# Kernel tuning notes

Measured on AMD Instinct MI355X. Metric: run time of the kernel, lower is better.

Reference implementation:

```python
import jax, jax.numpy as jnp
import numpy as np

N_NODES = 20000
N_EDGES = 640000
IN_DIM = 256
HID = 128
N_GRAPHS = 64


def setup_inputs() -> dict:
    key = jax.random.key(0)
    ks = jax.random.split(key, 9)
    x = jax.random.normal(ks[0], (N_NODES, IN_DIM), jnp.float32)
    edge_index = jax.random.randint(ks[1], (2, N_EDGES), 0, N_NODES, dtype=jnp.int32)
    batch = jnp.sort(jax.random.randint(ks[2], (N_NODES,), 0, N_GRAPHS, dtype=jnp.int32))

    def lin(k, fan_in, fan_out):
        # torch.nn.Linear default init: U(-1/sqrt(fan_in), 1/sqrt(fan_in))
        bound = 1.0 / np.sqrt(fan_in)
        kw, kb = jax.random.split(k)
        W = jax.random.uniform(kw, (fan_in, fan_out), jnp.float32, -bound, bound)
        b = jax.random.uniform(kb, (fan_out,), jnp.float32, -bound, bound)
        return W, b

    W0, b0 = lin(ks[3], IN_DIM, HID)
    W1, b1 = lin(ks[4], HID, HID)
    W2, b2 = lin(ks[5], HID, HID)
    return dict(x=x, edge_index=edge_index, batch=batch,
                W0=W0, b0=b0, W1=W1, b1=b1, W2=W2, b2=b2)


def reference(x, edge_index, batch, W0, b0, W1, b1, W2, b2):
    src, dst = edge_index[0], edge_index[1]
    edge_batch = batch[src]  # [E] segment id per edge
    ones = jnp.ones((edge_batch.shape[0], 1), x.dtype)
    counts = jax.ops.segment_sum(ones, edge_batch, num_segments=N_GRAPHS)
    inv_counts = 1.0 / jnp.maximum(counts, 1.0)

    def pool(z):
        # gather endpoint features, concat -> [E, 2*HID], mean pool by graph
        edge_emb = jnp.concatenate([z[src], z[dst]], axis=1)
        return jax.ops.segment_sum(edge_emb, edge_batch, num_segments=N_GRAPHS) * inv_counts

    g = []
    z = x
    for W, b in ((W0, b0), (W1, b1), (W2, b2)):
        z = z @ W + b
        g.append(pool(z))
    return jnp.concatenate(g, axis=1)  # [N_GRAPHS, 3 * 2 * HID]
```

## Files before the change

kernel.cpp:

```cpp
#include <hip/hip_runtime.h>

#define N_NODES 20000
#define N_EDGES 640000
#define N_GRAPHS 64

#define NCHUNK 128
#define CHUNK_SZ 157
#define GSPLIT 8
#define GSUB 8

#define BG_TILE 2048
#define NBG 313
#define SEGCAP 80
#define GR_CAP 768
#define NSLOT4 (NBG * SEGCAP / 4)

#define CD_OFF      0
#define DEG_OFF     1280000
#define CNT_OFF     1300000
#define Y_OFF       1300064
#define PART_OFF    1316448
#define BH_OFF      3413600
#define VALS_OFF    3433632

__global__ __launch_bounds__(256) void bucket_g_k(const int* __restrict__ ei,
                                                  const int* __restrict__ batch,
                                                  unsigned* __restrict__ vals,
                                                  unsigned* __restrict__ bh,
                                                  float* __restrict__ Y) {
    __shared__ unsigned hist[N_GRAPHS];
    const int t = threadIdx.x;
    const int blk = blockIdx.x;
    if (t < N_GRAPHS) hist[t] = 0u;
    __syncthreads();

    const int e0 = blk * BG_TILE;
    unsigned pv[8], rnk[8], gg[8];
#pragma unroll
    for (int k = 0; k < 8; ++k) {
        int e = e0 + t + k * 256;
        if (e < N_EDGES) {
            unsigned s = (unsigned)ei[e];
            unsigned d = (unsigned)ei[N_EDGES + e];
            unsigned g = (unsigned)batch[s];
            pv[k] = (s << 15) | d;
            gg[k] = g;
            rnk[k] = atomicAdd(&hist[g], 1u);
        } else {
            gg[k] = 0xFFFFFFFFu;
        }
    }
#pragma unroll
    for (int k = 0; k < 8; ++k) {
        unsigned g = gg[k];
        if (g != 0xFFFFFFFFu && rnk[k] < SEGCAP)
            vals[((size_t)g * NBG + blk) * SEGCAP + rnk[k]] = pv[k];
    }
    __syncthreads();
    if (t < N_GRAPHS) {
        unsigned c = hist[t];
        bh[blk * N_GRAPHS + t] = (c > SEGCAP) ? SEGCAP : c;
    }
    if (blk == 0) {
        float4* y4 = (float4*)Y;
        for (int i = t; i < 64 * 64; i += 256) y4[i] = make_float4(0.f, 0.f, 0.f, 0.f);
    }
}

__global__ __launch_bounds__(1024) void cd_col_k(const unsigned* __restrict__ vals,
                                                 const unsigned* __restrict__ bh,
                                                 const int* __restrict__ batch,
                                                 float* __restrict__ Cdcol,
                                                 float* __restrict__ deg,
                                                 float* __restrict__ counts) {
    __shared__ unsigned scnt[NBG];
    __shared__ unsigned dh[N_NODES / 2];
    __shared__ unsigned sdeg[GR_CAP];
    __shared__ int s_lo, s_hi;
    __shared__ unsigned stot;
    const int t = threadIdx.x;
    const int g = blockIdx.x;

    for (int i = t; i < N_NODES / 2; i += 1024) dh[i] = 0u;
    if (t < NBG) scnt[t] = bh[t * N_GRAPHS + g];
    if (t < GR_CAP) sdeg[t] = 0u;
    if (t == 0) {
        stot = 0u;
        int lo = 0, hi = N_NODES;
        while (lo < hi) { int m = (lo + hi) >> 1; if (batch[m] < g) lo = m + 1; else hi = m; }
        s_lo = lo;
        int lo2 = lo; hi = N_NODES;
        while (lo2 < hi) { int m = (lo2 + hi) >> 1; if (batch[m] < g + 1) lo2 = m + 1; else hi = m; }
        s_hi = lo2;
    }
    __syncthreads();
    const int lo = s_lo;

    const uint4* v4 = (const uint4*)(vals + (size_t)g * NBG * SEGCAP);
    for (int i = t; i < NSLOT4; i += 1024) {
        uint4 v = *(v4 + i);
        unsigned w = (unsigned)i * 4u;
        unsigned seg = (unsigned)(((unsigned long long)w * 53687092ull) >> 32);
        unsigned local = w - seg * 80u;
        unsigned c = scnt[seg];
#define CD_ONE(VX, L)                                                        \
        if ((L) < c) {                                                       \
            unsigned d_ = (VX) & 0x7FFFu;                                    \
            atomicAdd(&dh[d_ >> 1], 1u << ((d_ & 1u) * 16));                 \
            int rs_ = (int)((VX) >> 15) - lo;                                \
            if ((unsigned)rs_ < (unsigned)GR_CAP) atomicAdd(&sdeg[rs_], 1u); \
        }
        CD_ONE(v.x, local + 0u)
        CD_ONE(v.y, local + 1u)
        CD_ONE(v.z, local + 2u)
        CD_ONE(v.w, local + 3u)
#undef CD_ONE
    }
    if (t < NBG && scnt[t]) atomicAdd(&stot, scnt[t]);
    __syncthreads();

    float2* outc = (float2*)(Cdcol + (size_t)g * N_NODES);
    for (int w = t; w < N_NODES / 2; w += 1024) {
        unsigned v = dh[w];
        outc[w] = make_float2((float)(v & 0xFFFFu), (float)(v >> 16));
    }
    const int range = s_hi - lo;
    for (int i = t; i < range; i += 1024) deg[lo + i] = (float)sdeg[i];
    if (t == 0) counts[g] = (float)stot;
}

#define FMA8(C0, C1, XV)                                          \
    acc[0].x = fmaf(C0.x, XV.x, acc[0].x); acc[0].y = fmaf(C0.x, XV.y, acc[0].y); \
    acc[0].z = fmaf(C0.x, XV.z, acc[0].z); acc[0].w = fmaf(C0.x, XV.w, acc[0].w); \
    acc[1].x = fmaf(C0.y, XV.x, acc[1].x); acc[1].y = fmaf(C0.y, XV.y, acc[1].y); \
    acc[1].z = fmaf(C0.y, XV.z, acc[1].z); acc[1].w = fmaf(C0.y, XV.w, acc[1].w); \
    acc[2].x = fmaf(C0.z, XV.x, acc[2].x); acc[2].y = fmaf(C0.z, XV.y, acc[2].y); \
    acc[2].z = fmaf(C0.z, XV.z, acc[2].z); acc[2].w = fmaf(C0.z, XV.w, acc[2].w); \
    acc[3].x = fmaf(C0.w, XV.x, acc[3].x); acc[3].y = fmaf(C0.w, XV.y, acc[3].y); \
    acc[3].z = fmaf(C0.w, XV.z, acc[3].z); acc[3].w = fmaf(C0.w, XV.w, acc[3].w); \
    acc[4].x = fmaf(C1.x, XV.x, acc[4].x); acc[4].y = fmaf(C1.x, XV.y, acc[4].y); \
    acc[4].z = fmaf(C1.x, XV.z, acc[4].z); acc[4].w = fmaf(C1.x, XV.w, acc[4].w); \
    acc[5].x = fmaf(C1.y, XV.x, acc[5].x); acc[5].y = fmaf(C1.y, XV.y, acc[5].y); \
    acc[5].z = fmaf(C1.y, XV.z, acc[5].z); acc[5].w = fmaf(C1.y, XV.w, acc[5].w); \
    acc[6].x = fmaf(C1.z, XV.x, acc[6].x); acc[6].y = fmaf(C1.z, XV.y, acc[6].y); \
    acc[6].z = fmaf(C1.z, XV.z, acc[6].z); acc[6].w = fmaf(C1.z, XV.w, acc[6].w); \
    acc[7].x = fmaf(C1.w, XV.x, acc[7].x); acc[7].y = fmaf(C1.w, XV.y, acc[7].y); \
    acc[7].z = fmaf(C1.w, XV.z, acc[7].z); acc[7].w = fmaf(C1.w, XV.w, acc[7].w);

__global__ __launch_bounds__(256) void pool_k(const float* __restrict__ x,
                                              const int* __restrict__ batch,
                                              const float* __restrict__ Cdcol,
                                              const float* __restrict__ deg,
                                              float* __restrict__ Y,
                                              float* __restrict__ part) {
    __shared__ float4 sc4[CHUNK_SZ * 2];
    __shared__ float sdeg[CHUNK_SZ];
    __shared__ int   sbatch[CHUNK_SZ];
    __shared__ float4 red[2 * GSUB * 64];

    const int t = threadIdx.x;
    const int fg = t & 63;
    const int p  = t >> 6;
    const int b = blockIdx.x & 127;
    const int j = blockIdx.x >> 7;
    const int n0 = b * CHUNK_SZ;
    const int cnt = (n0 + CHUNK_SZ <= N_NODES) ? CHUNK_SZ : (N_NODES - n0);

    float* sc = (float*)sc4;
    const float* cbase = Cdcol + (size_t)(j * GSUB) * N_NODES + n0;
#pragma unroll
    for (int k = 0; k < GSUB; ++k)
        for (int i = t; i < cnt; i += 256)
            sc[i * GSUB + k] = cbase[(size_t)k * N_NODES + i];
    if (j == 0) {
        for (int i = t; i < cnt; i += 256) {
            sdeg[i] = deg[n0 + i];
            sbatch[i] = batch[n0 + i];
        }
    }
    __syncthreads();

    const float4* x4 = (const float4*)x;
    float4 acc[GSUB];
#pragma unroll
    for (int k = 0; k < GSUB; ++k) acc[k] = make_float4(0.f, 0.f, 0.f, 0.f);

    if (j == 0) {
        float4 accs = make_float4(0.f, 0.f, 0.f, 0.f);
        int gprev = (p < cnt) ? sbatch[p] : 0;
        int i = p;
        float4 xn = make_float4(0.f, 0.f, 0.f, 0.f);
        if (i < cnt) xn = x4[(size_t)(n0 + i) * 64 + fg];
        for (; i < cnt; i += 4) {
            float4 xv = xn;
            if (i + 4 < cnt) xn = x4[(size_t)(n0 + i + 4) * 64 + fg];
            int g = sbatch[i];
            if (g != gprev) {
                float* yr = Y + gprev * 256 + fg * 4;
                atomicAdd(yr + 0, accs.x); atomicAdd(yr + 1, accs.y);
                atomicAdd(yr + 2, accs.z); atomicAdd(yr + 3, accs.w);
                accs = make_float4(0.f, 0.f, 0.f, 0.f);
                gprev = g;
            }
            float dg = sdeg[i];
            accs.x = fmaf(dg, xv.x, accs.x); accs.y = fmaf(dg, xv.y, accs.y);
            accs.z = fmaf(dg, xv.z, accs.z); accs.w = fmaf(dg, xv.w, accs.w);
            float4 c0 = sc4[i * 2], c1 = sc4[i * 2 + 1];
            FMA8(c0, c1, xv)
        }
        if (p < cnt) {
            float* yr = Y + gprev * 256 + fg * 4;
            atomicAdd(yr + 0, accs.x); atomicAdd(yr + 1, accs.y);
            atomicAdd(yr + 2, accs.z); atomicAdd(yr + 3, accs.w);
        }
    } else {
        int i = p;
        float4 xn = make_float4(0.f, 0.f, 0.f, 0.f);
        if (i < cnt) xn = x4[(size_t)(n0 + i) * 64 + fg];
        for (; i < cnt; i += 4) {
            float4 xv = xn;
            if (i + 4 < cnt) xn = x4[(size_t)(n0 + i + 4) * 64 + fg];
            float4 c0 = sc4[i * 2], c1 = sc4[i * 2 + 1];
            FMA8(c0, c1, xv)
        }
    }

    if (p >= 2) {
#pragma unroll
        for (int k = 0; k < GSUB; ++k) red[(p - 2) * (GSUB * 64) + k * 64 + fg] = acc[k];
    }
    __syncthreads();
    if (p < 2) {
#pragma unroll
        for (int k = 0; k < GSUB; ++k) {
            float4 v = red[p * (GSUB * 64) + k * 64 + fg];
            acc[k].x += v.x; acc[k].y += v.y; acc[k].z += v.z; acc[k].w += v.w;
        }
    }
    __syncthreads();
    if (p == 1) {
#pragma unroll
        for (int k = 0; k < GSUB; ++k) red[k * 64 + fg] = acc[k];
    }
    __syncthreads();
    if (p == 0) {
        float4* part4 = (float4*)part;
#pragma unroll
        for (int k = 0; k < GSUB; ++k) {
            float4 v = red[k * 64 + fg];
            acc[k].x += v.x; acc[k].y += v.y; acc[k].z += v.z; acc[k].w += v.w;
            part4[(size_t)(b * 64 + j * GSUB + k) * 64 + fg] = acc[k];
        }
    }
}

__global__ __launch_bounds__(256) void chain2_k(const float* __restrict__ Y,
                                                const float* __restrict__ part,
                                                const float* __restrict__ counts,
                                                const float* __restrict__ W0, const float* __restrict__ b0,
                                                const float* __restrict__ W1, const float* __restrict__ b1,
                                                const float* __restrict__ W2, const float* __restrict__ b2,
                                                float* __restrict__ out) {
    __shared__ float m[256];
    __shared__ float h[128];
    const int r = blockIdx.x;
    const int t = threadIdx.x;
    const int g = r & 63;
    const int half = (r >= 64) ? 128 : 0;

    float c = counts[g];
    float inv = 1.0f / fmaxf(c, 1.0f);
    float beta = c * inv;

    if (r < 64) {
        m[t] = Y[r * 256 + t] * inv;
    } else {
        float s = 0.0f;
        for (int bb = 0; bb < NCHUNK; ++bb) s += part[(size_t)(bb * 64 + g) * 256 + t];
        m[t] = s * inv;
    }
    __syncthreads();

    if (t < 128) {
        float s1 = 0.0f;
        for (int k = 0; k < 256; ++k) s1 += m[k] * W0[k * 128 + t];
        s1 += beta * b0[t];
        out[g * 768 + 0 + half + t] = s1;
        h[t] = s1;
    }
    __syncthreads();
    float s2 = 0.0f;
    if (t < 128) {
        for (int k = 0; k < 128; ++k) s2 += h[k] * W1[k * 128 + t];
        s2 += beta * b1[t];
        out[g * 768 + 256 + half + t] = s2;
    }
    __syncthreads();
    if (t < 128) h[t] = s2;
    __syncthreads();
    if (t < 128) {
        float s3 = 0.0f;
        for (int k = 0; k < 128; ++k) s3 += h[k] * W2[k * 128 + t];
        s3 += beta * b2[t];
        out[g * 768 + 512 + half + t] = s3;
    }
}

extern "C" void kernel_launch(void* const* d_in, const int* in_sizes, int n_in,
                              void* d_out, int out_size, void* d_ws, size_t ws_size,
                              hipStream_t stream) {
    const float* x     = (const float*)d_in[0];
    const int*   ei    = (const int*)d_in[1];
    const int*   batch = (const int*)d_in[2];
    const float* W0    = (const float*)d_in[3];
    const float* b0    = (const float*)d_in[4];
    const float* W1    = (const float*)d_in[5];
    const float* b1    = (const float*)d_in[6];
    const float* W2    = (const float*)d_in[7];
    const float* b2    = (const float*)d_in[8];
    float* out = (float*)d_out;

    float*    ws     = (float*)d_ws;
    float*    Cdcol  = ws + CD_OFF;
    float*    deg    = ws + DEG_OFF;
    float*    counts = ws + CNT_OFF;
    float*    Y      = ws + Y_OFF;
    float*    part   = ws + PART_OFF;
    unsigned* bh     = (unsigned*)(ws + BH_OFF);
    unsigned* vals   = (unsigned*)(ws + VALS_OFF);

    bucket_g_k<<<NBG, 256, 0, stream>>>(ei, batch, vals, bh, Y);
    cd_col_k<<<N_GRAPHS, 1024, 0, stream>>>(vals, bh, batch, Cdcol, deg, counts);
    pool_k<<<NCHUNK * GSPLIT, 256, 0, stream>>>(x, batch, Cdcol, deg, Y, part);
    chain2_k<<<128, 256, 0, stream>>>(Y, part, counts, W0, b0, W1, b1, W2, b2, out);
}
```

Baseline: 129.4 us.

## Split degree histogram across node quarters, stage bucket writes in LDS, unroll pool loads

The per-graph column-degree kernel now runs four blocks per graph, each counting only a quarter of destination nodes. This shrinks shared memory per block and raises parallelism from 64 to 256 blocks, at the cost of each block rereading the graph's whole edge list. The bucketing kernel first sorts edges by graph in shared memory and then writes them out contiguously per segment, so the global stores are coalesced instead of scattered. The non-first pool path also unrolls by four, keeping more x loads in flight.

```diff
diff --git a/kernel.cpp b/kernel.cpp
--- a/kernel.cpp
+++ b/kernel.cpp
@@ -29,19 +29,22 @@
                                                   unsigned* __restrict__ bh,
                                                   float* __restrict__ Y) {
     __shared__ unsigned hist[N_GRAPHS];
+    __shared__ unsigned base[N_GRAPHS + 1];
+    __shared__ unsigned lv[BG_TILE];
     const int t = threadIdx.x;
     const int blk = blockIdx.x;
     if (t < N_GRAPHS) hist[t] = 0u;
     __syncthreads();
 
     const int e0 = blk * BG_TILE;
+    const int ecnt = (e0 + BG_TILE <= N_EDGES) ? BG_TILE : (N_EDGES - e0);
     unsigned pv[8], rnk[8], gg[8];
 #pragma unroll
     for (int k = 0; k < 8; ++k) {
-        int e = e0 + t + k * 256;
-        if (e < N_EDGES) {
-            unsigned s = (unsigned)ei[e];
-            unsigned d = (unsigned)ei[N_EDGES + e];
+        int i = t + k * 256;
+        if (i < ecnt) {
+            unsigned s = (unsigned)ei[e0 + i];
+            unsigned d = (unsigned)ei[N_EDGES + e0 + i];
             unsigned g = (unsigned)batch[s];
             pv[k] = (s << 15) | d;
             gg[k] = g;
@@ -50,16 +53,28 @@
             gg[k] = 0xFFFFFFFFu;
         }
     }
-#pragma unroll
-    for (int k = 0; k < 8; ++k) {
-        unsigned g = gg[k];
-        if (g != 0xFFFFFFFFu && rnk[k] < SEGCAP)
-            vals[((size_t)g * NBG + blk) * SEGCAP + rnk[k]] = pv[k];
-    }
-    __syncthreads();
+    __syncthreads();
+    if (t == 0) {
+        unsigned acc = 0u;
+        base[0] = 0u;
+        for (int g = 0; g < N_GRAPHS; ++g) { acc += hist[g]; base[g + 1] = acc; }
+    }
     if (t < N_GRAPHS) {
         unsigned c = hist[t];
         bh[blk * N_GRAPHS + t] = (c > SEGCAP) ? SEGCAP : c;
+    }
+    __syncthreads();
+#pragma unroll
+    for (int k = 0; k < 8; ++k) {
+        if (gg[k] != 0xFFFFFFFFu) lv[base[gg[k]] + rnk[k]] = pv[k];
+    }
+    __syncthreads();
+    for (int i = t; i < ecnt; i += 256) {
+        int lo = 0, hi = N_GRAPHS - 1;
+        while (lo < hi) { int m = (lo + hi + 1) >> 1; if (base[m] <= (unsigned)i) lo = m; else hi = m - 1; }
+        unsigned slot = (unsigned)i - base[lo];
+        if (slot < SEGCAP)
+            vals[((size_t)lo * NBG + blk) * SEGCAP + slot] = lv[i];
     }
     if (blk == 0) {
         float4* y4 = (float4*)Y;
@@ -74,27 +89,29 @@
                                                  float* __restrict__ deg,
                                                  float* __restrict__ counts) {
     __shared__ unsigned scnt[NBG];
-    __shared__ unsigned dh[N_NODES / 2];
+    __shared__ unsigned dh[2500];
     __shared__ unsigned sdeg[GR_CAP];
     __shared__ int s_lo, s_hi;
-    __shared__ unsigned stot;
     const int t = threadIdx.x;
-    const int g = blockIdx.x;
-
-    for (int i = t; i < N_NODES / 2; i += 1024) dh[i] = 0u;
+    const int g = blockIdx.x >> 2;
+    const int q = blockIdx.x & 3;
+    const int d0 = q * 5000;
+
+    for (int i = t; i < 2500; i += 1024) dh[i] = 0u;
     if (t < NBG) scnt[t] = bh[t * N_GRAPHS + g];
-    if (t < GR_CAP) sdeg[t] = 0u;
-    if (t == 0) {
-        stot = 0u;
-        int lo = 0, hi = N_NODES;
-        while (lo < hi) { int m = (lo + hi) >> 1; if (batch[m] < g) lo = m + 1; else hi = m; }
-        s_lo = lo;
-        int lo2 = lo; hi = N_NODES;
-        while (lo2 < hi) { int m = (lo2 + hi) >> 1; if (batch[m] < g + 1) lo2 = m + 1; else hi = m; }
-        s_hi = lo2;
-    }
-    __syncthreads();
-    const int lo = s_lo;
+    if (q == 0) {
+        if (t < GR_CAP) sdeg[t] = 0u;
+        if (t == 0) {
+            int lo = 0, hi = N_NODES;
+            while (lo < hi) { int m = (lo + hi) >> 1; if (batch[m] < g) lo = m + 1; else hi = m; }
+            s_lo = lo;
+            int lo2 = lo; hi = N_NODES;
+            while (lo2 < hi) { int m = (lo2 + hi) >> 1; if (batch[m] < g + 1) lo2 = m + 1; else hi = m; }
+            s_hi = lo2;
+        }
+    }
+    __syncthreads();
+    const int lo = (q == 0) ? s_lo : 0;
 
     const uint4* v4 = (const uint4*)(vals + (size_t)g * NBG * SEGCAP);
     for (int i = t; i < NSLOT4; i += 1024) {
@@ -103,12 +120,15 @@
         unsigned seg = (unsigned)(((unsigned long long)w * 53687092ull) >> 32);
         unsigned local = w - seg * 80u;
         unsigned c = scnt[seg];
-#define CD_ONE(VX, L)                                                        \
-        if ((L) < c) {                                                       \
-            unsigned d_ = (VX) & 0x7FFFu;                                    \
-            atomicAdd(&dh[d_ >> 1], 1u << ((d_ & 1u) * 16));                 \
-            int rs_ = (int)((VX) >> 15) - lo;                                \
-            if ((unsigned)rs_ < (unsigned)GR_CAP) atomicAdd(&sdeg[rs_], 1u); \
+#define CD_ONE(VX, L)                                                            \
+        if ((L) < c) {                                                           \
+            int rd_ = (int)((VX) & 0x7FFFu) - d0;                                \
+            if ((unsigned)rd_ < 5000u)                                           \
+                atomicAdd(&dh[rd_ >> 1], 1u << ((rd_ & 1) * 16));                \
+            if (q == 0) {                                                        \
+                int rs_ = (int)((VX) >> 15) - lo;                                \
+                if ((unsigned)rs_ < (unsigned)GR_CAP) atomicAdd(&sdeg[rs_], 1u); \
+            }                                                                    \
         }
         CD_ONE(v.x, local + 0u)
         CD_ONE(v.y, local + 1u)
@@ -116,17 +136,22 @@
         CD_ONE(v.w, local + 3u)
 #undef CD_ONE
     }
-    if (t < NBG && scnt[t]) atomicAdd(&stot, scnt[t]);
-    __syncthreads();
-
-    float2* outc = (float2*)(Cdcol + (size_t)g * N_NODES);
-    for (int w = t; w < N_NODES / 2; w += 1024) {
+    __syncthreads();
+
+    float2* outc = (float2*)(Cdcol + (size_t)g * N_NODES + d0);
+    for (int w = t; w < 2500; w += 1024) {
         unsigned v = dh[w];
         outc[w] = make_float2((float)(v & 0xFFFFu), (float)(v >> 16));
     }
-    const int range = s_hi - lo;
-    for (int i = t; i < range; i += 1024) deg[lo + i] = (float)sdeg[i];
-    if (t == 0) counts[g] = (float)stot;
+    if (q == 0) {
+        const int range = s_hi - lo;
+        for (int i = t; i < range; i += 1024) deg[lo + i] = (float)sdeg[i];
+        if (t == 0) {
+            unsigned tot = 0;
+            for (int i = 0; i < NBG; ++i) tot += scnt[i];
+            counts[g] = (float)tot;
+        }
+    }
 }
 
 #define FMA8(C0, C1, XV)                                          \
@@ -180,7 +205,8 @@
     }
     __syncthreads();
 
-    const float4* x4 = (const float4*)x;
+    const float4* xp = (const float4*)x + (size_t)n0 * 64 + fg;
+#define XL(I) xp[(size_t)(I) * 64]
     float4 acc[GSUB];
 #pragma unroll
     for (int k = 0; k < GSUB; ++k) acc[k] = make_float4(0.f, 0.f, 0.f, 0.f);
@@ -190,10 +216,10 @@
         int gprev = (p < cnt) ? sbatch[p] : 0;
         int i = p;
         float4 xn = make_float4(0.f, 0.f, 0.f, 0.f);
-        if (i < cnt) xn = x4[(size_t)(n0 + i) * 64 + fg];
+        if (i < cnt) xn = XL(i);
         for (; i < cnt; i += 4) {
             float4 xv = xn;
-            if (i + 4 < cnt) xn = x4[(size_t)(n0 + i + 4) * 64 + fg];
+            if (i + 4 < cnt) xn = XL(i + 4);
             int g = sbatch[i];
             if (g != gprev) {
                 float* yr = Y + gprev * 256 + fg * 4;
@@ -215,15 +241,41 @@
         }
     } else {
         int i = p;
-        float4 xn = make_float4(0.f, 0.f, 0.f, 0.f);
-        if (i < cnt) xn = x4[(size_t)(n0 + i) * 64 + fg];
+        float4 xa, xb, xc, xd;
+        if (i      < cnt) xa = XL(i);
+        if (i + 4  < cnt) xb = XL(i + 4);
+        if (i + 8  < cnt) xc = XL(i + 8);
+        if (i + 12 < cnt) xd = XL(i + 12);
+        for (; i + 12 < cnt; i += 16) {
+            float4 y0 = xa, y1 = xb, y2 = xc, y3 = xd;
+            if (i + 16 < cnt) xa = XL(i + 16);
+            if (i + 20 < cnt) xb = XL(i + 20);
+            if (i + 24 < cnt) xc = XL(i + 24);
+            if (i + 28 < cnt) xd = XL(i + 28);
+            {
+                float4 c0 = sc4[i * 2], c1 = sc4[i * 2 + 1];
+                FMA8(c0, c1, y0)
+            }
+            {
+                float4 c0 = sc4[(i + 4) * 2], c1 = sc4[(i + 4) * 2 + 1];
+                FMA8(c0, c1, y1)
+            }
+            {
+                float4 c0 = sc4[(i + 8) * 2], c1 = sc4[(i + 8) * 2 + 1];
+                FMA8(c0, c1, y2)
+            }
+            {
+                float4 c0 = sc4[(i + 12) * 2], c1 = sc4[(i + 12) * 2 + 1];
+                FMA8(c0, c1, y3)
+            }
+        }
         for (; i < cnt; i += 4) {
-            float4 xv = xn;
-            if (i + 4 < cnt) xn = x4[(size_t)(n0 + i + 4) * 64 + fg];
+            float4 xv = XL(i);
             float4 c0 = sc4[i * 2], c1 = sc4[i * 2 + 1];
             FMA8(c0, c1, xv)
         }
     }
+#undef XL
 
     if (p >= 2) {
 #pragma unroll
@@ -330,7 +382,7 @@
     unsigned* vals   = (unsigned*)(ws + VALS_OFF);
 
     bucket_g_k<<<NBG, 256, 0, stream>>>(ei, batch, vals, bh, Y);
-    cd_col_k<<<N_GRAPHS, 1024, 0, stream>>>(vals, bh, batch, Cdcol, deg, counts);
+    cd_col_k<<<N_GRAPHS * 4, 1024, 0, stream>>>(vals, bh, batch, Cdcol, deg, counts);
     pool_k<<<NCHUNK * GSPLIT, 256, 0, stream>>>(x, batch, Cdcol, deg, Y, part);
     chain2_k<<<128, 256, 0, stream>>>(Y, part, counts, W0, b0, W1, b1, W2, b2, out);
 }
```

Measured after the change: 127.7 us. About the same (-1.3%).
